# Kernel optimization log

Measured on AMD Instinct MI355X. Metric: run time of the kernel, lower is better.

The kernel has to match this reference:

```python
import jax, jax.numpy as jnp
import numpy as np

B, M, HWIN = 1024, 5, 25          # batch, encoder window, decoder horizon
SH, SW, HID = 64, 128, 256        # saliency map H/W, hidden size
SAL = SH * SW


def setup_inputs() -> dict:
    key = jax.random.key(0)
    ks = jax.random.split(key, 32)
    s = 0.02
    W = lambda k, shp: (jax.random.normal(k, shp, jnp.float32) * s)
    inp = {
        "enc_pos": jax.random.normal(ks[0], (B, M, 3), jnp.float32),
        "enc_sal": jax.random.uniform(ks[1], (B, M, SH, SW), jnp.float32),
        "dec_pos": jax.random.normal(ks[2], (B, 1, 3), jnp.float32),
        "dec_sal": jax.random.uniform(ks[3], (B, HWIN, SH, SW), jnp.float32),
        # fc_pos_enc / fc_sal_enc
        "Wpe": W(ks[4], (3, HID)),    "bpe": W(ks[5], (HID,)),
        "Wse": W(ks[6], (SAL, HID)),  "bse": W(ks[7], (HID,)),
        # fuse_1_enc LSTM (gate order i,f,g,o like torch)
        "Wih_e": W(ks[8], (2 * HID, 4 * HID)), "Whh_e": W(ks[9], (HID, 4 * HID)),
        "bih_e": W(ks[10], (4 * HID,)),        "bhh_e": W(ks[11], (4 * HID,)),
        # fuse_1_dec LSTM
        "Wih_d": W(ks[12], (2 * HID, 4 * HID)), "Whh_d": W(ks[13], (HID, 4 * HID)),
        "bih_d": W(ks[14], (4 * HID,)),         "bhh_d": W(ks[15], (4 * HID,)),
        # fc_pos_dec / fc_sal_dec
        "Wpd": W(ks[16], (3, HID)),   "bpd": W(ks[17], (HID,)),
        "Wsd": W(ks[18], (SAL, HID)), "bsd": W(ks[19], (HID,)),
        # fuse_2 and fc_layer_out
        "W2": W(ks[20], (HID, HID)),  "b2": W(ks[21], (HID,)),
        "Wo": W(ks[22], (HID, 3)),    "bo": W(ks[23], (3,)),
    }
    return inp


def _lstm_cell(h, c, x, Wih, Whh, b):
    g = x @ Wih + h @ Whh + b                     # [B, 4H]
    i, f, gg, o = jnp.split(g, 4, axis=-1)        # torch gate order i,f,g,o
    c = jax.nn.sigmoid(f) * c + jax.nn.sigmoid(i) * jnp.tanh(gg)
    h = jax.nn.sigmoid(o) * jnp.tanh(c)
    return h, c


def reference(enc_pos, enc_sal, dec_pos, dec_sal,
              Wpe, bpe, Wse, bse, Wih_e, Whh_e, bih_e, bhh_e,
              Wih_d, Whh_d, bih_d, bhh_d, Wpd, bpd, Wsd, bsd,
              W2, b2, Wo, bo):
    b = enc_pos.shape[0]
    hid = Whh_e.shape[0]
    # ---- encoder: per-timestep linear features, then LSTM over M steps ----
    sal_e = enc_sal.reshape(b, enc_sal.shape[1], -1) @ Wse + bse   # [B,M,H]
    pos_e = enc_pos @ Wpe + bpe                                     # [B,M,H]
    x_e = jnp.concatenate([sal_e, pos_e], axis=-1)                  # [B,M,2H]
    be = bih_e + bhh_e

    h0 = jnp.zeros((b, hid), enc_pos.dtype)
    c0 = jnp.zeros((b, hid), enc_pos.dtype)

    def enc_step(carry, xt):
        h, c = carry
        h, c = _lstm_cell(h, c, xt, Wih_e, Whh_e, be)
        return (h, c), None

    (h, c), _ = jax.lax.scan(enc_step, (h0, c0), jnp.swapaxes(x_e, 0, 1))

    sal_d = dec_sal.reshape(b, dec_sal.shape[1], -1) @ Wsd + bsd    # [B,Hw,H]
    bd = bih_d + bhh_d

    def dec_step(carry, sal_t):
        h, c, pos = carry                       # pos: [B,3]
        pf = pos @ Wpd + bpd                    # fc_pos_dec
        x = jnp.concatenate([sal_t, pf], axis=-1)
        h, c = _lstm_cell(h, c, x, Wih_d, Whh_d, bd)
        delta = (h @ W2 + b2) @ Wo + bo         # fuse_2 -> fc_layer_out
        newpos = pos + delta                    # toPosition: add delta,
        newpos = newpos / jnp.linalg.norm(newpos, axis=-1, keepdims=True)
        return (h, c, newpos), newpos

    pos0 = dec_pos[:, 0, :]
    _, outs = jax.lax.scan(dec_step, (h, c, pos0), jnp.swapaxes(sal_d, 0, 1))
    return jnp.swapaxes(outs, 0, 1)             # [B, H_WINDOW, 3]
```

## Files before the change

### kernel.cpp

```cpp
#include <hip/hip_runtime.h>

typedef _Float16 f16;
typedef _Float16 f16x4 __attribute__((ext_vector_type(4)));
typedef _Float16 f16x8 __attribute__((ext_vector_type(8)));
typedef float    f32x4 __attribute__((ext_vector_type(4)));
typedef int      i32x4 __attribute__((ext_vector_type(4)));
typedef unsigned int u32;

#define MFMA16(a,b,c) __builtin_amdgcn_mfma_f32_16x16x32_f16((a),(b),(c),0,0,0)
#define MFMAI8(a,b,c) __builtin_amdgcn_mfma_i32_16x16x64_i8((a),(b),(c),0,0,0)

typedef __attribute__((address_space(1))) const u32 gu32;
typedef __attribute__((address_space(3))) u32 lu32;

static __device__ __forceinline__ float frcp(float x){ float r; asm("v_rcp_f32 %0, %1" : "=v"(r) : "v"(x)); return r; }
static __device__ __forceinline__ float frsq(float x){ float r; asm("v_rsq_f32 %0, %1" : "=v"(r) : "v"(x)); return r; }
static __device__ __forceinline__ float sigm(float x){ return frcp(1.0f + __expf(-x)); }
static __device__ __forceinline__ float tanh_(float x){ return 1.0f - 2.0f*frcp(1.0f + __expf(2.0f*x)); }

static __device__ __forceinline__ void bar_lgkm(){
  asm volatile("s_waitcnt lgkmcnt(0)" ::: "memory");
  __builtin_amdgcn_s_barrier();
  asm volatile("" ::: "memory");
}
static __device__ __forceinline__ void bar_plain(){
  asm volatile("" ::: "memory");
  __builtin_amdgcn_s_barrier();
  asm volatile("" ::: "memory");
}

static constexpr size_t OFF_WSE_P  = 0;
static constexpr size_t OFF_WSD_P  = OFF_WSE_P  + (size_t)8192*256*2;
static constexpr size_t OFF_WIHE_P = OFF_WSD_P  + (size_t)8192*256*2;
static constexpr size_t OFF_WIHD_P = OFF_WIHE_P + (size_t)256*1024*2;
static constexpr size_t OFF_WHHE_P = OFF_WIHD_P + (size_t)256*1024*2;
static constexpr size_t OFF_WHHD_P = OFF_WHHE_P + (size_t)256*1024;
static constexpr size_t OFF_W3E    = OFF_WHHD_P + (size_t)256*1024;
static constexpr size_t OFF_W3D    = OFF_W3E   + (size_t)3*1024*4;
static constexpr size_t OFF_W2WO   = OFF_W3D   + (size_t)3*1024*4;
static constexpr size_t OFF_BIASE  = OFF_W2WO  + (size_t)256*3*4;
static constexpr size_t OFF_BIASD  = OFF_BIASE + (size_t)1024*4;
static constexpr size_t OFF_B2WO   = OFF_BIASD + (size_t)1024*4;
static constexpr size_t OFF_PREGE  = OFF_B2WO  + 256;
static constexpr size_t OFF_PREGD  = OFF_PREGE + (size_t)5120*1024*2;
static constexpr size_t OFF_END    = OFF_PREGD + (size_t)25600*1024*2;

__global__ __launch_bounds__(256) void k_prep(
    const float* __restrict__ Wse, const float* __restrict__ Wsd,
    const float* __restrict__ Wih_e, const float* __restrict__ Wih_d,
    const float* __restrict__ Whh_e, const float* __restrict__ Whh_d,
    f16* pWse, f16* pWsd, f16* pWih_e, f16* pWih_d,
    signed char* pWhh_e, signed char* pWhh_d,
    const float* __restrict__ Wpe, const float* __restrict__ bpe,
    const float* __restrict__ bih_e, const float* __restrict__ bhh_e,
    const float* __restrict__ Wpd, const float* __restrict__ bpd,
    const float* __restrict__ bih_d, const float* __restrict__ bhh_d,
    const float* __restrict__ W2, const float* __restrict__ b2,
    const float* __restrict__ Wo, const float* __restrict__ bo,
    float* W3e, float* W3d, float* biasE, float* biasD, float* W2Wo, float* b2Wo)
{
  int blk = blockIdx.x;
  if (blk < 2304) {
    const float* W; f16* o; int N, base;
    if      (blk < 1024) { W=Wse;   o=pWse;   N=256;  base=0; }
    else if (blk < 2048) { W=Wsd;   o=pWsd;   N=256;  base=1024; }
    else if (blk < 2176) { W=Wih_e; o=pWih_e; N=1024; base=2048; }
    else                 { W=Wih_d; o=pWih_d; N=1024; base=2176; }
    int tid = (blk - base)*256 + threadIdx.x;
    int l = tid & 63;
    int nct = N >> 4;
    int ctg = (tid >> 6) % nct;
    int kfg = (tid >> 6) / nct;
    int k0  = kfg*32 + ((l>>4)<<3);
    int col = ctg*16 + (l&15);
    f16x8 v;
#pragma unroll
    for (int i=0;i<8;++i) v[i] = (f16)W[(size_t)(k0+i)*N + col];
    *(f16x8*)(o + (size_t)tid*8) = v;
    return;
  }
  if (blk < 2432) {
    const float* W; signed char* o; int base;
    if (blk < 2368) { W=Whh_e; o=pWhh_e; base=2304; }
    else            { W=Whh_d; o=pWhh_d; base=2368; }
    int tid = (blk - base)*256 + threadIdx.x;
    int l = tid & 63;
    int unit = tid >> 6;
    int kfg = unit >> 6, ctg = unit & 63;
    int k0  = kfg*64 + ((l>>4)<<4);
    int col = ctg*16 + (l&15);
    signed char* dst = o + ((size_t)unit*64 + l)*16;
#pragma unroll
    for (int e=0;e<16;++e) {
      int q = __float2int_rn(W[(size_t)(k0+e)*1024 + col] * 1024.0f);
      q = q > 127 ? 127 : (q < -127 ? -127 : q);
      dst[e] = (signed char)q;
    }
    return;
  }
  int bid = blk - 2432, tid = threadIdx.x;
  if (bid < 4) {
    int j = bid*256 + tid;
    float s0=0,s1=0,s2=0,sb=0;
    for (int m=0;m<256;++m) {
      float wv = Wih_e[(size_t)(256+m)*1024 + j];
      s0 += Wpe[m]*wv; s1 += Wpe[256+m]*wv; s2 += Wpe[512+m]*wv; sb += bpe[m]*wv;
    }
    W3e[j]=s0; W3e[1024+j]=s1; W3e[2048+j]=s2;
    biasE[j] = bih_e[j] + bhh_e[j] + sb;
  } else if (bid < 8) {
    int j = (bid-4)*256 + tid;
    float s0=0,s1=0,s2=0,sb=0;
    for (int m=0;m<256;++m) {
      float wv = Wih_d[(size_t)(256+m)*1024 + j];
      s0 += Wpd[m]*wv; s1 += Wpd[256+m]*wv; s2 += Wpd[512+m]*wv; sb += bpd[m]*wv;
    }
    W3d[j]=s0; W3d[1024+j]=s1; W3d[2048+j]=s2;
    biasD[j] = bih_d[j] + bhh_d[j] + sb;
  } else if (bid == 8) {
    int c = tid;
    float s0=0,s1=0,s2=0;
    for (int m=0;m<256;++m) {
      float wv = W2[(size_t)c*256+m];
      s0 += wv*Wo[m*3+0]; s1 += wv*Wo[m*3+1]; s2 += wv*Wo[m*3+2];
    }
    W2Wo[c*3+0]=s0; W2Wo[c*3+1]=s1; W2Wo[c*3+2]=s2;
  } else {
    if (tid < 192) {
      int j = tid >> 6, lane = tid & 63;
      float s = 0.f;
      for (int m=lane;m<256;m+=64) s += b2[m]*Wo[m*3+j];
#pragma unroll
      for (int msk=1;msk<64;msk<<=1) s += __shfl_xor(s, msk);
      if (lane==0) b2Wo[j] = s + bo[j];
    }
  }
}

__global__ __launch_bounds__(256) void k_gemm_fused(
    const float* __restrict__ A0, const f16* __restrict__ W0,
    const float* __restrict__ bs0, const f16* __restrict__ Wih0,
    const float* __restrict__ bias0, f16* __restrict__ P0, int nb0, int T0,
    const float* __restrict__ pos0, const float* __restrict__ W3f0,
    const float* __restrict__ A1, const f16* __restrict__ W1,
    const float* __restrict__ bs1, const f16* __restrict__ Wih1,
    const float* __restrict__ bias1, f16* __restrict__ P1, int T1)
{
  __shared__ f16 aLDS[2][64*64];
  __shared__ f16 sLDS[64*256];
  const int tid = threadIdx.x, l = tid & 63, w = tid >> 6;
  const int li = l & 15, hi = l >> 4;
  const int bx = blockIdx.x;
  const float *Ap, *bs, *bias, *posf, *W3f; const f16 *Wp, *Wih; f16* P; int rblk, T;
  if (bx < nb0) { Ap=A0; Wp=W0; bs=bs0; Wih=Wih0; bias=bias0; P=P0; rblk=bx*64;       T=T0; posf=pos0; W3f=W3f0; }
  else          { Ap=A1; Wp=W1; bs=bs1; Wih=Wih1; bias=bias1; P=P1; rblk=(bx-nb0)*64; T=T1; posf=nullptr; W3f=nullptr; }
  const int t = rblk >> 10, b0 = rblk & 1023;

  f32x4 acc[4][4];
#pragma unroll
  for (int a=0;a<4;++a)
#pragma unroll
    for (int b=0;b<4;++b) acc[a][b] = (f32x4){0.f,0.f,0.f,0.f};

  const int srow = tid >> 2, kseg = tid & 3;
  const float* Arow = Ap + ((size_t)(b0 + srow)*T + t)*8192 + kseg*16;

  float4 fA0,fA1,fA2,fA3, fB0,fB1,fB2,fB3;
#define LOADA_A(ti_) { const float* Aq = Arow + (ti_)*64;                      \
    fA0 = *(const float4*)Aq;     fA1 = *(const float4*)(Aq+4);                \
    fA2 = *(const float4*)(Aq+8); fA3 = *(const float4*)(Aq+12); }
#define LOADA_B(ti_) { const float* Aq = Arow + (ti_)*64;                      \
    fB0 = *(const float4*)Aq;     fB1 = *(const float4*)(Aq+4);                \
    fB2 = *(const float4*)(Aq+8); fB3 = *(const float4*)(Aq+12); }
#define MFMA_TILE(buf_, kfg0_)                                                 \
  _Pragma("unroll")                                                            \
  for (int kf = 0; kf < 2; ++kf) {                                             \
    f16x8 afr[4], bfr[4];                                                      \
    _Pragma("unroll")                                                          \
    for (int rt=0; rt<4; ++rt) {                                               \
      int row = rt*16 + li;                                                    \
      afr[rt] = *(f16x8*)&aLDS[buf_][row*64 + (((kf*4) + hi) ^ (row&7))*8];    \
    }                                                                          \
    _Pragma("unroll")                                                          \
    for (int ct=0; ct<4; ++ct) {                                               \
      int ctg = w*4 + ct;                                                      \
      bfr[ct] = *(const f16x8*)(Wp + ((size_t)(((kfg0_)+kf)*16 + ctg)*64 + l)*8); \
    }                                                                          \
    _Pragma("unroll")                                                          \
    for (int rt=0; rt<4; ++rt)                                                 \
      _Pragma("unroll")                                                        \
      for (int ct=0; ct<4; ++ct)                                               \
        acc[rt][ct] = MFMA16(afr[rt], bfr[ct], acc[rt][ct]);                   \
  }
#define STAGE1_STEP(F0,F1,F2,F3, RELOAD, buf_, ti_) {                          \
    f16x8 w0, w1;               \
    w0[0]=(f16)F0.x; w0[1]=(f16)F0.y; w0[2]=(f16)F0.z; w0[3]=(f16)F0.w;        \
    w0[4]=(f16)F1.x; w0[5]=(f16)F1.y; w0[6]=(f16)F1.z; w0[7]=(f16)F1.w;        \
    w1[0]=(f16)F2.x; w1[1]=(f16)F2.y; w1[2]=(f16)F2.z; w1[3]=(f16)F2.w;        \
    w1[4]=(f16)F3.x; w1[5]=(f16)F3.y; w1[6]=(f16)F3.z; w1[7]=(f16)F3.w;        \
    bar_plain();                     \
    *(f16x8*)&aLDS[buf_][srow*64 + ((kseg*2    ) ^ (srow&7))*8] = w0;          \
    *(f16x8*)&aLDS[buf_][srow*64 + ((kseg*2 + 1) ^ (srow&7))*8] = w1;          \
    { int tn = ((ti_)+2 < 128) ? (ti_)+2 : 127; RELOAD(tn); }                  \
    bar_lgkm();                       \
    MFMA_TILE(buf_, (ti_)*2)                                                   \
  }

  LOADA_A(0); LOADA_B(1);
  for (int ti = 0; ti < 128; ti += 2) {
    STAGE1_STEP(fA0,fA1,fA2,fA3, LOADA_A, 0, ti)
    STAGE1_STEP(fB0,fB1,fB2,fB3, LOADA_B, 1, ti+1)
  }
#undef LOADA_A
#undef LOADA_B
#undef MFMA_TILE
#undef STAGE1_STEP
  bar_plain();
#pragma unroll
  for (int ct=0; ct<4; ++ct) {
    int col = (w*4 + ct)*16 + li;
    float bv = bs[col];
    int slot = col >> 3;
#pragma unroll
    for (int rt=0; rt<4; ++rt)
#pragma unroll
      for (int i=0;i<4;++i) {
        int row = rt*16 + hi*4 + i;
        sLDS[row*256 + ((slot ^ (row&7))<<3) + (col&7)] = (f16)(acc[rt][ct][i] + bv);
      }
  }
  float pe[4][4][3];
  if (posf) {
#pragma unroll
    for (int rt=0; rt<4; ++rt)
#pragma unroll
      for (int i=0;i<4;++i) {
        int brow = b0 + rt*16 + hi*4 + i;
        const float* pq = posf + ((size_t)brow*T + t)*3;
        pe[rt][i][0]=pq[0]; pe[rt][i][1]=pq[1]; pe[rt][i][2]=pq[2];
      }
  }
  __syncthreads();
  const int bblk0 = b0 >> 4;
#pragma unroll
  for (int cg=0; cg<4; ++cg) {
    f32x4 a2[4][4];
#pragma unroll
    for (int a=0;a<4;++a)
#pragma unroll
      for (int b=0;b<4;++b) a2[a][b] = (f32x4){0.f,0.f,0.f,0.f};
#pragma unroll
    for (int kfg=0; kfg<8; ++kfg) {
      f16x8 afr[4], bfr[4];
#pragma unroll
      for (int rt=0; rt<4; ++rt) {
        int row = rt*16 + li;
        afr[rt] = *(f16x8*)&sLDS[row*256 + (((kfg*4 + hi) ^ (row&7))<<3)];
      }
#pragma unroll
      for (int ct=0; ct<4; ++ct) {
        int ctg2 = cg*16 + w*4 + ct;
        bfr[ct] = *(const f16x8*)(Wih + ((size_t)(kfg*64 + ctg2)*64 + l)*8);
      }
#pragma unroll
      for (int rt=0; rt<4; ++rt)
#pragma unroll
        for (int ct=0; ct<4; ++ct)
          a2[rt][ct] = MFMA16(afr[rt], bfr[ct], a2[rt][ct]);
    }
#pragma unroll
    for (int ct=0; ct<4; ++ct) {
      const int ctg2 = cg*16 + w*4 + ct;
      const float bv = bias[ctg2*16 + li];
      float w30=0.f, w31=0.f, w32=0.f;
      if (posf) { int gc = ctg2*16 + li; w30=W3f[gc]; w31=W3f[1024+gc]; w32=W3f[2048+gc]; }
#pragma unroll
      for (int rt=0; rt<4; ++rt) {
        f16x4 o;
#pragma unroll
        for (int i=0;i<4;++i) {
          float v = a2[rt][ct][i] + bv;
          if (posf) v += pe[rt][i][0]*w30 + pe[rt][i][1]*w31 + pe[rt][i][2]*w32;
          o[i] = (f16)v;
        }
        *(f16x4*)(P + ((size_t)((bblk0 + rt)*T + t)*64 + ctg2)*256 + l*4) = o;
      }
    }
  }
}

__global__ __launch_bounds__(512) void k_rnn(
    const f16* __restrict__ pregE,
    const f16* __restrict__ pregD,
    const signed char* __restrict__ Whh_e_p, const signed char* __restrict__ Whh_d_p,
    const float* __restrict__ W3d, const float* __restrict__ dec_pos,
    const float* __restrict__ W2Wo, const float* __restrict__ b2Wo,
    float* __restrict__ out)
{
  __shared__ signed char wLDS[8][4][4][1024];
  __shared__ signed char hBuf[2][16*256];
  __shared__ f16 W3h[3*1024];
  __shared__ float dpart[25][16][3];
  const int tid = threadIdx.x, l = tid & 63, w = tid >> 6;
  const int li = l & 15, hi = l >> 4;
  const int bblk = blockIdx.x, rb = bblk*16;
  const float SC = 1.0f/130048.0f;

  for (int i=tid;i<3072;i+=512) W3h[i] = (f16)W3d[i];
  for (int i=tid; i<25*16*3; i+=512) ((float*)dpart)[i] = 0.f;

  float c_st[2][4];
#pragma unroll
  for (int j=0;j<2;++j)
#pragma unroll
    for (int i=0;i<4;++i) c_st[j][i]=0.f;

#define VMW(n) { asm volatile("s_waitcnt vmcnt(" #n ")" ::: "memory");        \
                 __builtin_amdgcn_sched_barrier(0); }
#define STAGE(WP, kf, h, s)                                                   \
  _Pragma("unroll") for (int f=0; f<4; ++f) {                                 \
    int ctg = ((h)*2 + (f>>1))*16 + w*2 + (f&1);                              \
    const signed char* g = (WP) + ((size_t)((kf)*64 + ctg)*64 + l)*16;        \
    __builtin_amdgcn_global_load_lds((gu32*)g, (lu32*)&wLDS[w][s][f][0], 16, 0, 0); \
  }
#define AH(ah, hB, kf) ah = *(i32x4*)&(hB)[li*256 + ((((kf)*4)+hi) ^ (li&7))*16];
#define MFMA4(s, h, ah)                                                       \
  _Pragma("unroll") for (int f=0; f<4; ++f) {                                 \
    i32x4 b = *(i32x4*)&wLDS[w][s][f][l*16];                                  \
    acc[(h)*2 + (f>>1)][f&1] = MFMAI8(ah, b, acc[(h)*2 + (f>>1)][f&1]); }
#define KFSTREAM8(hB, WP, WPn, PVB, PVT) {                                    \
  i32x4 ah;                                                                   \
  VMW(8) AH(ah, hB, 0) MFMA4(0, 0, ah) STAGE(WP, 1, 1, 3)                     \
  VMW(8)               MFMA4(1, 1, ah) STAGE(WP, 2, 0, 0)                     \
  VMW(8) AH(ah, hB, 1) MFMA4(2, 0, ah) STAGE(WP, 2, 1, 1)                     \
  VMW(8)               MFMA4(3, 1, ah) STAGE(WP, 3, 0, 2)                     \
  VMW(8) AH(ah, hB, 2) MFMA4(0, 0, ah) STAGE(WP, 3, 1, 3)                     \
  VMW(8)               MFMA4(1, 1, ah) LOADPV(pvB, PVB, PVT) STAGE(WPn, 0, 0, 0) \
  VMW(24) AH(ah, hB, 3) MFMA4(2, 0, ah) STAGE(WPn, 0, 1, 1)                   \
  VMW(24)               MFMA4(3, 1, ah) STAGE(WPn, 1, 0, 2)                   \
  }
#define LOADPV(dst, base, t_)                                                 \
  _Pragma("unroll")                                                           \
  for (int q=0;q<4;++q)                                                       \
    _Pragma("unroll")                                                         \
    for (int j=0;j<2;++j)                                                     \
      dst[q][j] = *(const f16x4*)((base) + ((size_t)(t_)*16384 + (size_t)(q*16 + w*2 + j)*256 + l*4));
#define COPYPV()                                                              \
  _Pragma("unroll")                                                           \
  for (int q=0;q<4;++q)                                                       \
    _Pragma("unroll")                                                         \
    for (int j=0;j<2;++j) pvA[q][j] = pvB[q][j];
#define ACCZERO()                                                             \
  i32x4 acc[4][2];                                                            \
  _Pragma("unroll")                                                           \
  for (int q=0;q<4;++q)                                                       \
    _Pragma("unroll")                                                         \
    for (int j=0;j<2;++j) acc[q][j] = (i32x4){0,0,0,0};
#define HWRITE(hB, r, hc, hval)                                               \
  (hB)[(r)*256 + ((((hc)>>4) ^ ((r)&7))<<4) + ((hc)&15)] =                    \
      (signed char)__float2int_rn((hval)*127.0f);

  const f16* prE = pregE + (size_t)bblk*5*16384;
  const f16* prD = pregD + (size_t)bblk*25*16384;
  f16x4 pvA[4][2], pvB[4][2];

  __syncthreads();
  LOADPV(pvA, prE, 0)
  STAGE(Whh_e_p,0,0,0) STAGE(Whh_e_p,0,1,1) STAGE(Whh_e_p,1,0,2)

  for (int t=0;t<5;++t) {
    ACCZERO()
    if (t > 0) {
      if (t < 4) { KFSTREAM8(hBuf[(t-1)&1], Whh_e_p, Whh_e_p, prE, t+1) }
      else       { KFSTREAM8(hBuf[(t-1)&1], Whh_e_p, Whh_d_p, prD, 0)   }
    }
#pragma unroll
    for (int i=0;i<4;++i) {
      int r = hi*4 + i;
#pragma unroll
      for (int j=0;j<2;++j) {
        int hc = w*32 + j*16 + li;
        float gq[4];
#pragma unroll
        for (int q=0;q<4;++q)
          gq[q] = (float)pvA[q][j][i] + (float)acc[q][j][i]*SC;
        float cn = sigm(gq[1])*c_st[j][i] + sigm(gq[0])*tanh_(gq[2]);
        c_st[j][i] = cn;
        float h = sigm(gq[3])*tanh_(cn);
        HWRITE(hBuf[t&1], r, hc, h)
      }
    }
    if (t == 0) LOADPV(pvB, prE, 1)
    COPYPV()
    bar_lgkm();
  }

  float w2r[2][3];
#pragma unroll
  for (int j=0;j<2;++j) {
    int hc = w*32 + j*16 + li;
    w2r[j][0]=W2Wo[hc*3+0]; w2r[j][1]=W2Wo[hc*3+1]; w2r[j][2]=W2Wo[hc*3+2];
  }
  const float b2w0 = b2Wo[0], b2w1 = b2Wo[1], b2w2 = b2Wo[2];
  float pp[4][3];
#pragma unroll
  for (int i=0;i<4;++i) {
    int r = rb + hi*4 + i;
    pp[i][0]=dec_pos[r*3+0]; pp[i][1]=dec_pos[r*3+1]; pp[i][2]=dec_pos[r*3+2];
  }

  for (int t=0;t<25;++t) {
    ACCZERO()
    if (t+1 < 25) { KFSTREAM8(hBuf[t&1], Whh_d_p, Whh_d_p, prD, t+1) }
    else          { KFSTREAM8(hBuf[t&1], Whh_d_p, Whh_d_p, prD, 24)  }
    float w3v[2][4][3];
#pragma unroll
    for (int j=0;j<2;++j)
#pragma unroll
      for (int q=0;q<4;++q) {
        int gc = q*256 + w*32 + j*16 + li;
        w3v[j][q][0] = (float)W3h[gc];
        w3v[j][q][1] = (float)W3h[1024+gc];
        w3v[j][q][2] = (float)W3h[2048+gc];
      }
    float dpar[4][3];
#pragma unroll
    for (int i=0;i<4;++i){ dpar[i][0]=0.f; dpar[i][1]=0.f; dpar[i][2]=0.f; }
#pragma unroll
    for (int i=0;i<4;++i) {
      int r = hi*4 + i;
#pragma unroll
      for (int j=0;j<2;++j) {
        int hc = w*32 + j*16 + li;
        float gq[4];
#pragma unroll
        for (int q=0;q<4;++q)
          gq[q] = (float)pvA[q][j][i] + (float)acc[q][j][i]*SC
                + pp[i][0]*w3v[j][q][0] + pp[i][1]*w3v[j][q][1] + pp[i][2]*w3v[j][q][2];
        float cn = sigm(gq[1])*c_st[j][i] + sigm(gq[0])*tanh_(gq[2]);
        c_st[j][i] = cn;
        float h = sigm(gq[3])*tanh_(cn);
        HWRITE(hBuf[(t+1)&1], r, hc, h)
        dpar[i][0] += h*w2r[j][0];
        dpar[i][1] += h*w2r[j][1];
        dpar[i][2] += h*w2r[j][2];
      }
    }
#pragma unroll
    for (int m=1;m<16;m<<=1)
#pragma unroll
      for (int i=0;i<4;++i) {
        dpar[i][0] += __shfl_xor(dpar[i][0], m);
        dpar[i][1] += __shfl_xor(dpar[i][1], m);
        dpar[i][2] += __shfl_xor(dpar[i][2], m);
      }
    if (li==0) {
#pragma unroll
      for (int i=0;i<4;++i) {
        int r = hi*4 + i;
        atomicAdd(&dpart[t][r][0], dpar[i][0]);
        atomicAdd(&dpart[t][r][1], dpar[i][1]);
        atomicAdd(&dpart[t][r][2], dpar[i][2]);
      }
    }
    COPYPV()
    bar_lgkm();
#pragma unroll
    for (int i=0;i<4;++i) {
      int r = hi*4 + i;
      float p0 = pp[i][0] + b2w0 + dpart[t][r][0];
      float p1 = pp[i][1] + b2w1 + dpart[t][r][1];
      float p2 = pp[i][2] + b2w2 + dpart[t][r][2];
      float inv = frsq(p0*p0+p1*p1+p2*p2);
      pp[i][0]=p0*inv; pp[i][1]=p1*inv; pp[i][2]=p2*inv;
      if (w==0 && li==0) {
        float* o = out + (size_t)(rb+r)*75 + t*3;
        o[0]=pp[i][0]; o[1]=pp[i][1]; o[2]=pp[i][2];
      }
    }
  }
#undef VMW
#undef STAGE
#undef AH
#undef MFMA4
#undef KFSTREAM8
#undef LOADPV
#undef COPYPV
#undef ACCZERO
#undef HWRITE
}

extern "C" void kernel_launch(void* const* d_in, const int* in_sizes, int n_in,
                              void* d_out, int out_size, void* d_ws, size_t ws_size,
                              hipStream_t stream)
{
  const float* enc_pos = (const float*)d_in[0];
  const float* enc_sal = (const float*)d_in[1];
  const float* dec_pos = (const float*)d_in[2];
  const float* dec_sal = (const float*)d_in[3];
  const float* Wpe  = (const float*)d_in[4];
  const float* bpe  = (const float*)d_in[5];
  const float* Wse  = (const float*)d_in[6];
  const float* bse  = (const float*)d_in[7];
  const float* Wih_e= (const float*)d_in[8];
  const float* Whh_e= (const float*)d_in[9];
  const float* bih_e= (const float*)d_in[10];
  const float* bhh_e= (const float*)d_in[11];
  const float* Wih_d= (const float*)d_in[12];
  const float* Whh_d= (const float*)d_in[13];
  const float* bih_d= (const float*)d_in[14];
  const float* bhh_d= (const float*)d_in[15];
  const float* Wpd  = (const float*)d_in[16];
  const float* bpd  = (const float*)d_in[17];
  const float* Wsd  = (const float*)d_in[18];
  const float* bsd  = (const float*)d_in[19];
  const float* W2   = (const float*)d_in[20];
  const float* b2   = (const float*)d_in[21];
  const float* Wo   = (const float*)d_in[22];
  const float* bo   = (const float*)d_in[23];

  char* ws = (char*)d_ws;
  f16* pWse   = (f16*)(ws + OFF_WSE_P);
  f16* pWsd   = (f16*)(ws + OFF_WSD_P);
  f16* pWih_e = (f16*)(ws + OFF_WIHE_P);
  f16* pWih_d = (f16*)(ws + OFF_WIHD_P);
  signed char* pWhh_e = (signed char*)(ws + OFF_WHHE_P);
  signed char* pWhh_d = (signed char*)(ws + OFF_WHHD_P);
  float* W3e  = (float*)(ws + OFF_W3E);
  float* W3d  = (float*)(ws + OFF_W3D);
  float* W2WoP= (float*)(ws + OFF_W2WO);
  float* biasE= (float*)(ws + OFF_BIASE);
  float* biasD= (float*)(ws + OFF_BIASD);
  float* b2WoP= (float*)(ws + OFF_B2WO);
  f16* pregE  = (f16*)(ws + OFF_PREGE);
  f16* pregD  = (f16*)(ws + OFF_PREGD);
  float* out  = (float*)d_out;

  hipLaunchKernelGGL(k_prep, dim3(2442), dim3(256), 0, stream,
                     Wse, Wsd, Wih_e, Wih_d, Whh_e, Whh_d,
                     pWse, pWsd, pWih_e, pWih_d, pWhh_e, pWhh_d,
                     Wpe, bpe, bih_e, bhh_e, Wpd, bpd, bih_d, bhh_d,
                     W2, b2, Wo, bo,
                     W3e, W3d, biasE, biasD, W2WoP, b2WoP);
  hipLaunchKernelGGL(k_gemm_fused, dim3(480), dim3(256), 0, stream,
                     enc_sal, pWse, bse, pWih_e, biasE, pregE, 80, 5, enc_pos, W3e,
                     dec_sal, pWsd, bsd, pWih_d, biasD, pregD, 25);
  hipLaunchKernelGGL(k_rnn, dim3(64), dim3(512), 0, stream,
                     pregE, pregD, pWhh_e, pWhh_d,
                     W3d, dec_pos, W2WoP, b2WoP, out);
}
```

Before: 505.5 us.

## Keep recurrent Whh weights resident in registers and LDS instead of streaming per step

The RNN kernel now runs 4 waves instead of 8. Each wave holds half of its int8 Whh slice in VGPRs (32 i32x4) and the other half in LDS, loaded once per phase, rather than re-streaming the weights from global memory every timestep through a staged pipeline. The W3 position weights also move from an f16 LDS copy into per-thread float registers, and the next pregate tile is prefetched at the start of each step. This removes the per-step global weight traffic and its vmcnt waits, at the cost of half as many waves for the gate math and much higher register pressure, which risks spills.

```diff
diff --git a/kernel.cpp b/kernel.cpp
--- a/kernel.cpp
+++ b/kernel.cpp
@@ -193,16 +193,16 @@
         acc[rt][ct] = MFMA16(afr[rt], bfr[ct], acc[rt][ct]);                   \
   }
 #define STAGE1_STEP(F0,F1,F2,F3, RELOAD, buf_, ti_) {                          \
-    f16x8 w0, w1;               \
+    f16x8 w0, w1;                                                              \
     w0[0]=(f16)F0.x; w0[1]=(f16)F0.y; w0[2]=(f16)F0.z; w0[3]=(f16)F0.w;        \
     w0[4]=(f16)F1.x; w0[5]=(f16)F1.y; w0[6]=(f16)F1.z; w0[7]=(f16)F1.w;        \
     w1[0]=(f16)F2.x; w1[1]=(f16)F2.y; w1[2]=(f16)F2.z; w1[3]=(f16)F2.w;        \
     w1[4]=(f16)F3.x; w1[5]=(f16)F3.y; w1[6]=(f16)F3.z; w1[7]=(f16)F3.w;        \
-    bar_plain();                     \
+    bar_plain();                                                               \
     *(f16x8*)&aLDS[buf_][srow*64 + ((kseg*2    ) ^ (srow&7))*8] = w0;          \
     *(f16x8*)&aLDS[buf_][srow*64 + ((kseg*2 + 1) ^ (srow&7))*8] = w1;          \
     { int tn = ((ti_)+2 < 128) ? (ti_)+2 : 127; RELOAD(tn); }                  \
-    bar_lgkm();                       \
+    bar_lgkm();                                                                \
     MFMA_TILE(buf_, (ti_)*2)                                                   \
   }
 
@@ -289,7 +289,7 @@
   }
 }
 
-__global__ __launch_bounds__(512) void k_rnn(
+__global__ __launch_bounds__(256, 1) void k_rnn(
     const f16* __restrict__ pregE,
     const f16* __restrict__ pregD,
     const signed char* __restrict__ Whh_e_p, const signed char* __restrict__ Whh_d_p,
@@ -297,109 +297,124 @@
     const float* __restrict__ W2Wo, const float* __restrict__ b2Wo,
     float* __restrict__ out)
 {
-  __shared__ signed char wLDS[8][4][4][1024];
+  __shared__ signed char pLDS[4][2][16][1024];
   __shared__ signed char hBuf[2][16*256];
-  __shared__ f16 W3h[3*1024];
   __shared__ float dpart[25][16][3];
   const int tid = threadIdx.x, l = tid & 63, w = tid >> 6;
   const int li = l & 15, hi = l >> 4;
   const int bblk = blockIdx.x, rb = bblk*16;
   const float SC = 1.0f/130048.0f;
 
-  for (int i=tid;i<3072;i+=512) W3h[i] = (f16)W3d[i];
-  for (int i=tid; i<25*16*3; i+=512) ((float*)dpart)[i] = 0.f;
-
-  float c_st[2][4];
-#pragma unroll
-  for (int j=0;j<2;++j)
+  for (int i=tid; i<25*16*3; i+=256) ((float*)dpart)[i] = 0.f;
+
+  float c_st[4][4];
+#pragma unroll
+  for (int j=0;j<4;++j)
 #pragma unroll
     for (int i=0;i<4;++i) c_st[j][i]=0.f;
 
-#define VMW(n) { asm volatile("s_waitcnt vmcnt(" #n ")" ::: "memory");        \
-                 __builtin_amdgcn_sched_barrier(0); }
-#define STAGE(WP, kf, h, s)                                                   \
-  _Pragma("unroll") for (int f=0; f<4; ++f) {                                 \
-    int ctg = ((h)*2 + (f>>1))*16 + w*2 + (f&1);                              \
-    const signed char* g = (WP) + ((size_t)((kf)*64 + ctg)*64 + l)*16;        \
-    __builtin_amdgcn_global_load_lds((gu32*)g, (lu32*)&wLDS[w][s][f][0], 16, 0, 0); \
-  }
-#define AH(ah, hB, kf) ah = *(i32x4*)&(hB)[li*256 + ((((kf)*4)+hi) ^ (li&7))*16];
-#define MFMA4(s, h, ah)                                                       \
-  _Pragma("unroll") for (int f=0; f<4; ++f) {                                 \
-    i32x4 b = *(i32x4*)&wLDS[w][s][f][l*16];                                  \
-    acc[(h)*2 + (f>>1)][f&1] = MFMAI8(ah, b, acc[(h)*2 + (f>>1)][f&1]); }
-#define KFSTREAM8(hB, WP, WPn, PVB, PVT) {                                    \
+  i32x4 wreg[32];
+
+#define LOADWREG(WP)                                                          \
+  _Pragma("unroll") for (int kk=0;kk<2;++kk)                                  \
+  _Pragma("unroll") for (int f=0;f<16;++f) {                                  \
+    int ctg = (f>>2)*16 + w*4 + (f&3);                                        \
+    wreg[kk*16+f] = *(const i32x4*)((WP) + ((size_t)(kk*64 + ctg)*64 + l)*16); \
+  }
+#define LOADWLDS(WP)                                                          \
+  _Pragma("unroll") for (int kk=0;kk<2;++kk)                                  \
+  _Pragma("unroll") for (int f=0;f<16;++f) {                                  \
+    int ctg = (f>>2)*16 + w*4 + (f&3);                                        \
+    const signed char* gp = (WP) + ((size_t)((kk+2)*64 + ctg)*64 + l)*16;     \
+    __builtin_amdgcn_global_load_lds((gu32*)gp, (lu32*)&pLDS[w][kk][f][0], 16, 0, 0); \
+  }
+#define AHK(ah, hB, kf) ah = *(i32x4*)&(hB)[li*256 + ((((kf)*4)+hi) ^ (li&7))*16];
+#define MFMA_ALL(hB) {                                                        \
   i32x4 ah;                                                                   \
-  VMW(8) AH(ah, hB, 0) MFMA4(0, 0, ah) STAGE(WP, 1, 1, 3)                     \
-  VMW(8)               MFMA4(1, 1, ah) STAGE(WP, 2, 0, 0)                     \
-  VMW(8) AH(ah, hB, 1) MFMA4(2, 0, ah) STAGE(WP, 2, 1, 1)                     \
-  VMW(8)               MFMA4(3, 1, ah) STAGE(WP, 3, 0, 2)                     \
-  VMW(8) AH(ah, hB, 2) MFMA4(0, 0, ah) STAGE(WP, 3, 1, 3)                     \
-  VMW(8)               MFMA4(1, 1, ah) LOADPV(pvB, PVB, PVT) STAGE(WPn, 0, 0, 0) \
-  VMW(24) AH(ah, hB, 3) MFMA4(2, 0, ah) STAGE(WPn, 0, 1, 1)                   \
-  VMW(24)               MFMA4(3, 1, ah) STAGE(WPn, 1, 0, 2)                   \
-  }
+  _Pragma("unroll") for (int kk=0;kk<2;++kk) {                                \
+    AHK(ah, hB, kk)                                                           \
+    _Pragma("unroll") for (int f=0;f<16;++f)                                  \
+      acc[f>>2][f&3] = MFMAI8(ah, wreg[kk*16+f], acc[f>>2][f&3]);             \
+  }                                                                           \
+  _Pragma("unroll") for (int kk=0;kk<2;++kk) {                                \
+    AHK(ah, hB, kk+2)                                                         \
+    _Pragma("unroll") for (int f=0;f<16;++f) {                                \
+      i32x4 b = *(i32x4*)&pLDS[w][kk][f][l*16];                               \
+      acc[f>>2][f&3] = MFMAI8(ah, b, acc[f>>2][f&3]);                         \
+    }                                                                         \
+  } }
 #define LOADPV(dst, base, t_)                                                 \
   _Pragma("unroll")                                                           \
   for (int q=0;q<4;++q)                                                       \
     _Pragma("unroll")                                                         \
-    for (int j=0;j<2;++j)                                                     \
-      dst[q][j] = *(const f16x4*)((base) + ((size_t)(t_)*16384 + (size_t)(q*16 + w*2 + j)*256 + l*4));
+    for (int jj=0;jj<4;++jj)                                                  \
+      dst[q][jj] = *(const f16x4*)((base) + ((size_t)(t_)*16384 + (size_t)(q*16 + w*4 + jj)*256 + l*4));
 #define COPYPV()                                                              \
   _Pragma("unroll")                                                           \
   for (int q=0;q<4;++q)                                                       \
     _Pragma("unroll")                                                         \
-    for (int j=0;j<2;++j) pvA[q][j] = pvB[q][j];
+    for (int jj=0;jj<4;++jj) pvA[q][jj] = pvB[q][jj];
 #define ACCZERO()                                                             \
-  i32x4 acc[4][2];                                                            \
+  i32x4 acc[4][4];                                                            \
   _Pragma("unroll")                                                           \
   for (int q=0;q<4;++q)                                                       \
     _Pragma("unroll")                                                         \
-    for (int j=0;j<2;++j) acc[q][j] = (i32x4){0,0,0,0};
+    for (int jj=0;jj<4;++jj) acc[q][jj] = (i32x4){0,0,0,0};
 #define HWRITE(hB, r, hc, hval)                                               \
   (hB)[(r)*256 + ((((hc)>>4) ^ ((r)&7))<<4) + ((hc)&15)] =                    \
       (signed char)__float2int_rn((hval)*127.0f);
+#define VMW0() { asm volatile("s_waitcnt vmcnt(0)" ::: "memory");             \
+                 __builtin_amdgcn_sched_barrier(0); }
 
   const f16* prE = pregE + (size_t)bblk*5*16384;
   const f16* prD = pregD + (size_t)bblk*25*16384;
-  f16x4 pvA[4][2], pvB[4][2];
-
+  f16x4 pvA[4][4], pvB[4][4];
+
+  LOADWLDS(Whh_e_p)
+  LOADWREG(Whh_e_p)
+  LOADPV(pvA, prE, 0)
+  VMW0()
   __syncthreads();
-  LOADPV(pvA, prE, 0)
-  STAGE(Whh_e_p,0,0,0) STAGE(Whh_e_p,0,1,1) STAGE(Whh_e_p,1,0,2)
 
   for (int t=0;t<5;++t) {
+    if (t+1 < 5) LOADPV(pvB, prE, t+1)
     ACCZERO()
-    if (t > 0) {
-      if (t < 4) { KFSTREAM8(hBuf[(t-1)&1], Whh_e_p, Whh_e_p, prE, t+1) }
-      else       { KFSTREAM8(hBuf[(t-1)&1], Whh_e_p, Whh_d_p, prD, 0)   }
-    }
+    if (t > 0) MFMA_ALL(hBuf[(t-1)&1])
 #pragma unroll
     for (int i=0;i<4;++i) {
       int r = hi*4 + i;
 #pragma unroll
-      for (int j=0;j<2;++j) {
-        int hc = w*32 + j*16 + li;
+      for (int jj=0;jj<4;++jj) {
+        int hc = w*64 + jj*16 + li;
         float gq[4];
 #pragma unroll
         for (int q=0;q<4;++q)
-          gq[q] = (float)pvA[q][j][i] + (float)acc[q][j][i]*SC;
-        float cn = sigm(gq[1])*c_st[j][i] + sigm(gq[0])*tanh_(gq[2]);
-        c_st[j][i] = cn;
+          gq[q] = (float)pvA[q][jj][i] + (float)acc[q][jj][i]*SC;
+        float cn = sigm(gq[1])*c_st[jj][i] + sigm(gq[0])*tanh_(gq[2]);
+        c_st[jj][i] = cn;
         float h = sigm(gq[3])*tanh_(cn);
         HWRITE(hBuf[t&1], r, hc, h)
       }
     }
-    if (t == 0) LOADPV(pvB, prE, 1)
-    COPYPV()
+    if (t+1 < 5) { COPYPV() }
     bar_lgkm();
   }
 
-  float w2r[2][3];
-#pragma unroll
-  for (int j=0;j<2;++j) {
-    int hc = w*32 + j*16 + li;
-    w2r[j][0]=W2Wo[hc*3+0]; w2r[j][1]=W2Wo[hc*3+1]; w2r[j][2]=W2Wo[hc*3+2];
+  LOADWLDS(Whh_d_p)
+  LOADWREG(Whh_d_p)
+  float w3r[4][4][3];
+#pragma unroll
+  for (int jj=0;jj<4;++jj)
+#pragma unroll
+    for (int q=0;q<4;++q) {
+      int gc = q*256 + w*64 + jj*16 + li;
+      w3r[jj][q][0]=W3d[gc]; w3r[jj][q][1]=W3d[1024+gc]; w3r[jj][q][2]=W3d[2048+gc];
+    }
+  float w2r[4][3];
+#pragma unroll
+  for (int jj=0;jj<4;++jj) {
+    int hc = w*64 + jj*16 + li;
+    w2r[jj][0]=W2Wo[hc*3+0]; w2r[jj][1]=W2Wo[hc*3+1]; w2r[jj][2]=W2Wo[hc*3+2];
   }
   const float b2w0 = b2Wo[0], b2w1 = b2Wo[1], b2w2 = b2Wo[2];
   float pp[4][3];
@@ -408,21 +423,13 @@
     int r = rb + hi*4 + i;
     pp[i][0]=dec_pos[r*3+0]; pp[i][1]=dec_pos[r*3+1]; pp[i][2]=dec_pos[r*3+2];
   }
+  LOADPV(pvA, prD, 0)
+  VMW0()
 
   for (int t=0;t<25;++t) {
+    if (t+1 < 25) LOADPV(pvB, prD, t+1)
     ACCZERO()
-    if (t+1 < 25) { KFSTREAM8(hBuf[t&1], Whh_d_p, Whh_d_p, prD, t+1) }
-    else          { KFSTREAM8(hBuf[t&1], Whh_d_p, Whh_d_p, prD, 24)  }
-    float w3v[2][4][3];
-#pragma unroll
-    for (int j=0;j<2;++j)
-#pragma unroll
-      for (int q=0;q<4;++q) {
-        int gc = q*256 + w*32 + j*16 + li;
-        w3v[j][q][0] = (float)W3h[gc];
-        w3v[j][q][1] = (float)W3h[1024+gc];
-        w3v[j][q][2] = (float)W3h[2048+gc];
-      }
+    MFMA_ALL(hBuf[t&1])
     float dpar[4][3];
 #pragma unroll
     for (int i=0;i<4;++i){ dpar[i][0]=0.f; dpar[i][1]=0.f; dpar[i][2]=0.f; }
@@ -430,20 +437,20 @@
     for (int i=0;i<4;++i) {
       int r = hi*4 + i;
 #pragma unroll
-      for (int j=0;j<2;++j) {
-        int hc = w*32 + j*16 + li;
+      for (int jj=0;jj<4;++jj) {
+        int hc = w*64 + jj*16 + li;
         float gq[4];
 #pragma unroll
         for (int q=0;q<4;++q)
-          gq[q] = (float)pvA[q][j][i] + (float)acc[q][j][i]*SC
-                + pp[i][0]*w3v[j][q][0] + pp[i][1]*w3v[j][q][1] + pp[i][2]*w3v[j][q][2];
-        float cn = sigm(gq[1])*c_st[j][i] + sigm(gq[0])*tanh_(gq[2]);
-        c_st[j][i] = cn;
+          gq[q] = (float)pvA[q][jj][i] + (float)acc[q][jj][i]*SC
+                + pp[i][0]*w3r[jj][q][0] + pp[i][1]*w3r[jj][q][1] + pp[i][2]*w3r[jj][q][2];
+        float cn = sigm(gq[1])*c_st[jj][i] + sigm(gq[0])*tanh_(gq[2]);
+        c_st[jj][i] = cn;
         float h = sigm(gq[3])*tanh_(cn);
         HWRITE(hBuf[(t+1)&1], r, hc, h)
-        dpar[i][0] += h*w2r[j][0];
-        dpar[i][1] += h*w2r[j][1];
-        dpar[i][2] += h*w2r[j][2];
+        dpar[i][0] += h*w2r[jj][0];
+        dpar[i][1] += h*w2r[jj][1];
+        dpar[i][2] += h*w2r[jj][2];
       }
     }
 #pragma unroll
@@ -463,7 +470,7 @@
         atomicAdd(&dpart[t][r][2], dpar[i][2]);
       }
     }
-    COPYPV()
+    if (t+1 < 25) { COPYPV() }
     bar_lgkm();
 #pragma unroll
     for (int i=0;i<4;++i) {
@@ -479,15 +486,15 @@
       }
     }
   }
-#undef VMW
-#undef STAGE
-#undef AH
-#undef MFMA4
-#undef KFSTREAM8
+#undef LOADWREG
+#undef LOADWLDS
+#undef AHK
+#undef MFMA_ALL
 #undef LOADPV
 #undef COPYPV
 #undef ACCZERO
 #undef HWRITE
+#undef VMW0
 }
 
 extern "C" void kernel_launch(void* const* d_in, const int* in_sizes, int n_in,
@@ -545,7 +552,7 @@
   hipLaunchKernelGGL(k_gemm_fused, dim3(480), dim3(256), 0, stream,
                      enc_sal, pWse, bse, pWih_e, biasE, pregE, 80, 5, enc_pos, W3e,
                      dec_sal, pWsd, bsd, pWih_d, biasD, pregD, 25);
-  hipLaunchKernelGGL(k_rnn, dim3(64), dim3(512), 0, stream,
+  hipLaunchKernelGGL(k_rnn, dim3(64), dim3(256), 0, stream,
                      pregE, pregD, pWhh_e, pWhh_d,
                      W3d, dec_pos, W2WoP, b2WoP, out);
 }
```

Result: slower. 522.8 us (+3.4%).
